# Performance work log

Measured on AMD Instinct MI355X. Metric: run time of the kernel, lower is better.

## Reference

```python
import jax, jax.numpy as jnp
import numpy as np

N_HEADS = 16
D_MODEL = 1024
HEAD_DIM = D_MODEL // N_HEADS
B, S = 2, 2048


def setup_inputs() -> dict:
    key = jax.random.key(0)
    ks = jax.random.split(key, 10)
    scale = 1.0 / np.sqrt(D_MODEL)
    inp = {
        "query_tokens": jax.random.normal(ks[0], (B, S, D_MODEL), dtype=jnp.float32),
        "key_or_value_tokens": jax.random.normal(ks[1], (B, S, D_MODEL), dtype=jnp.float32),
        "mask": jnp.ones((B, S, S), dtype=jnp.int32),
        "Wq": jax.random.normal(ks[2], (D_MODEL, D_MODEL), dtype=jnp.float32) * scale,
        "bq": jnp.zeros((D_MODEL,), dtype=jnp.float32),
        "Wk": jax.random.normal(ks[3], (D_MODEL, D_MODEL), dtype=jnp.float32) * scale,
        "bk": jnp.zeros((D_MODEL,), dtype=jnp.float32),
        "Wv": jax.random.normal(ks[4], (D_MODEL, D_MODEL), dtype=jnp.float32) * scale,
        "bv": jnp.zeros((D_MODEL,), dtype=jnp.float32),
        "Wo": jax.random.normal(ks[5], (D_MODEL, D_MODEL), dtype=jnp.float32) * scale,
        "bo": jnp.zeros((D_MODEL,), dtype=jnp.float32),
    }
    return inp


def reference(query_tokens, key_or_value_tokens, mask, Wq, bq, Wk, bk, Wv, bv, Wo, bo):
    b, s, d = query_tokens.shape
    h, dh = N_HEADS, HEAD_DIM

    def proj(x, W, bias):
        # torch Linear: x @ W.T + b ; then split heads -> (b, h, s, dh)
        y = jnp.einsum("bsd,ed->bse", x, W) + bias
        return y.reshape(b, -1, h, dh).transpose(0, 2, 1, 3)

    q = proj(query_tokens, Wq, bq)
    k = proj(key_or_value_tokens, Wk, bk)
    v = proj(key_or_value_tokens, Wv, bv)

    scores = jnp.einsum("bhqd,bhkd->bhqk", q, k) / jnp.sqrt(jnp.float32(dh))
    # mask: (b, Sq, Sk) -> (b, 1, Sq, Sk); zeros get large negative fill
    scores = jnp.where(mask[:, None, :, :] == 0, jnp.float32(-1e9), scores)
    attn = jax.nn.softmax(scores, axis=-1)
    out = jnp.einsum("bhqk,bhkd->bhqd", attn, v)
    out = out.transpose(0, 2, 1, 3).reshape(b, s, d)
    return jnp.einsum("bsd,ed->bse", out, Wo) + bo
```

## Files before the change

kernel.cpp:

```cpp
#include <hip/hip_runtime.h>
#include <hip/hip_bf16.h>

typedef __bf16 bf16_8  __attribute__((ext_vector_type(8)));
typedef __bf16 bf16_4  __attribute__((ext_vector_type(4)));
typedef float  f32_4   __attribute__((ext_vector_type(4)));

#define NH 16
#define DHD 64
#define BB 2
#define SS 2048
#define DD 1024

__device__ __forceinline__ void gload16(const __bf16* g, __bf16* l) {
    __builtin_amdgcn_global_load_lds(
        (const __attribute__((address_space(1))) void*)g,
        (__attribute__((address_space(3))) void*)l, 16, 0, 0);
}

__global__ __launch_bounds__(256) void conv_all(
    const float* __restrict__ s0, const float* __restrict__ s1,
    const float* __restrict__ s2, const float* __restrict__ s3,
    const float* __restrict__ s4, const float* __restrict__ s5,
    __bf16* __restrict__ d0, __bf16* __restrict__ d1, __bf16* __restrict__ d2,
    __bf16* __restrict__ d3, __bf16* __restrict__ d4, __bf16* __restrict__ d5) {
    const int y = blockIdx.y;
    if (y >= 2 && blockIdx.x >= 1024) return;
    const float* s = (y == 0) ? s0 : (y == 1) ? s1 : (y == 2) ? s2
                   : (y == 3) ? s3 : (y == 4) ? s4 : s5;
    __bf16* d      = (y == 0) ? d0 : (y == 1) ? d1 : (y == 2) ? d2
                   : (y == 3) ? d3 : (y == 4) ? d4 : d5;
    const int i = (blockIdx.x * 256 + threadIdx.x) * 4;
    f32_4 v = *(const f32_4*)&s[i];
    bf16_4 o; o[0] = (__bf16)v[0]; o[1] = (__bf16)v[1];
    o[2] = (__bf16)v[2]; o[3] = (__bf16)v[3];
    *(bf16_4*)&d[i] = o;
}

__global__ __launch_bounds__(256) void mask_flags_k(const int* __restrict__ mask,
                                                    int* __restrict__ flags) {
    const int id = blockIdx.x;
    const int b = id >> 10, qt = (id >> 5) & 31, kt = id & 31;
    const int t = threadIdx.x;
    const int row = t >> 2, seg = t & 3;
    const int* p = mask + ((size_t)b * SS + qt * 64 + row) * SS + kt * 64 + seg * 16;
    int any0 = 0;
#pragma unroll
    for (int i = 0; i < 4; ++i) {
        int4 v = *(const int4*)&p[i * 4];
        any0 |= (v.x == 0) | (v.y == 0) | (v.z == 0) | (v.w == 0);
    }
    unsigned long long bal = __ballot(any0);
    __shared__ int sf[4];
    if ((t & 63) == 0) sf[t >> 6] = (bal != 0ULL);
    __syncthreads();
    if (t == 0) flags[id] = sf[0] | sf[1] | sf[2] | sf[3];
}

template <int LAYOUT>
__device__ __forceinline__ void gemm_body(const __bf16* __restrict__ A,
                                          const __bf16* __restrict__ W,
                                          const float* __restrict__ bias,
                                          __bf16* __restrict__ out,
                                          __bf16* ldsA, __bf16* ldsB) {
    const int tid  = threadIdx.x;
    const int lane = tid & 63;
    const int w    = tid >> 6;
    const int quad = lane >> 4;
    const int l15  = lane & 15;
    const int wm   = (w >> 1) * 64;
    const int wn   = (w & 1) * 64;
    const int m0   = blockIdx.x * 128;
    const int n0   = blockIdx.y * 128;

    f32_4 acc[4][4] = {};

    for (int kt = 0; kt < 1024; kt += 32) {
#pragma unroll
        for (int cc = 0; cc < 2; ++cc) {
            const int c   = tid + cc * 256;
            const int row = c >> 2;
            const int cp  = c & 3;
            gload16(&A[(size_t)(m0 + row) * 1024 + kt + cp * 8], &ldsA[c * 8]);
            gload16(&W[(size_t)(n0 + row) * 1024 + kt + cp * 8], &ldsB[c * 8]);
        }
        __syncthreads();

        bf16_8 af[4], bfr[4];
#pragma unroll
        for (int i = 0; i < 4; ++i)
            af[i] = *(const bf16_8*)&ldsA[(wm + i * 16 + l15) * 32 + quad * 8];
#pragma unroll
        for (int j = 0; j < 4; ++j)
            bfr[j] = *(const bf16_8*)&ldsB[(wn + j * 16 + l15) * 32 + quad * 8];
#pragma unroll
        for (int i = 0; i < 4; ++i)
#pragma unroll
            for (int j = 0; j < 4; ++j)
                acc[i][j] = __builtin_amdgcn_mfma_f32_16x16x32_bf16(
                    af[i], bfr[j], acc[i][j], 0, 0, 0);
        __syncthreads();
    }

#pragma unroll
    for (int i = 0; i < 4; ++i) {
#pragma unroll
        for (int j = 0; j < 4; ++j) {
            const int col = n0 + wn + j * 16 + l15;
            const float bv = bias[col];
            if (LAYOUT == 2) {
                const int row0 = m0 + wm + i * 16 + quad * 4;
                bf16_4 pk;
#pragma unroll
                for (int r = 0; r < 4; ++r) pk[r] = (__bf16)(acc[i][j][r] + bv);
                const int bb = row0 >> 11, s0 = row0 & 2047;
                const int h = col >> 6, dh = col & 63;
                *(bf16_4*)&out[(((size_t)bb * NH + h) * DHD + dh) * SS + s0] = pk;
            } else {
#pragma unroll
                for (int r = 0; r < 4; ++r) {
                    const int row = m0 + wm + i * 16 + quad * 4 + r;
                    out[(((size_t)(row >> 11) * NH + (col >> 6)) * SS +
                         (row & 2047)) * DHD + (col & 63)] =
                        (__bf16)(acc[i][j][r] + bv);
                }
            }
        }
    }
}

__global__ __launch_bounds__(256) void gemm_qkv(
    const __bf16* __restrict__ Xq, const __bf16* __restrict__ Xkv,
    const __bf16* __restrict__ Wq, const float* __restrict__ bq,
    const __bf16* __restrict__ Wk, const float* __restrict__ bk,
    const __bf16* __restrict__ Wv, const float* __restrict__ bv,
    __bf16* __restrict__ Qo, __bf16* __restrict__ Ko, __bf16* __restrict__ VTo) {
    __shared__ __align__(16) __bf16 ldsA[128 * 32];
    __shared__ __align__(16) __bf16 ldsB[128 * 32];
    const int z = blockIdx.z;
    const __bf16* A    = (z == 0) ? Xq : Xkv;
    const __bf16* W    = (z == 0) ? Wq : (z == 1 ? Wk : Wv);
    const float* bias  = (z == 0) ? bq : (z == 1 ? bk : bv);
    if (z == 2)
        gemm_body<2>(A, W, bias, VTo, ldsA, ldsB);
    else
        gemm_body<0>(A, W, bias, (z == 0) ? Qo : Ko, ldsA, ldsB);
}

__global__ __launch_bounds__(256) void gemm_final(
    const __bf16* __restrict__ A, const __bf16* __restrict__ W,
    const float* __restrict__ bias, float* __restrict__ out) {
    __shared__ __align__(16) __bf16 ldsA[64 * 32];
    __shared__ __align__(16) __bf16 ldsB[64 * 32];
    const int tid  = threadIdx.x;
    const int lane = tid & 63;
    const int w    = tid >> 6;
    const int quad = lane >> 4;
    const int l15  = lane & 15;
    const int wm   = (w >> 1) * 32;
    const int wn   = (w & 1) * 32;
    const int m0   = blockIdx.x * 64;
    const int n0   = blockIdx.y * 64;

    const int isB = w >> 1;
    const __bf16* src = isB ? W : A;
    const int     bN  = isB ? n0 : m0;
    __bf16*       dst = isB ? ldsB : ldsA;
    const int     w2  = w & 1;

    f32_4 acc[2][2] = {};

    for (int kt = 0; kt < 1024; kt += 32) {
#pragma unroll
        for (int cc = 0; cc < 2; ++cc) {
            const int c   = w2 * 128 + cc * 64 + lane;
            const int row = c >> 2;
            const int cp  = c & 3;
            gload16(&src[(size_t)(bN + row) * 1024 + kt + cp * 8], &dst[c * 8]);
        }
        __syncthreads();

        bf16_8 af[2], bfr[2];
#pragma unroll
        for (int i = 0; i < 2; ++i)
            af[i] = *(const bf16_8*)&ldsA[(wm + i * 16 + l15) * 32 + quad * 8];
#pragma unroll
        for (int j = 0; j < 2; ++j)
            bfr[j] = *(const bf16_8*)&ldsB[(wn + j * 16 + l15) * 32 + quad * 8];
#pragma unroll
        for (int i = 0; i < 2; ++i)
#pragma unroll
            for (int j = 0; j < 2; ++j)
                acc[i][j] = __builtin_amdgcn_mfma_f32_16x16x32_bf16(
                    af[i], bfr[j], acc[i][j], 0, 0, 0);
        __syncthreads();
    }

#pragma unroll
    for (int i = 0; i < 2; ++i)
#pragma unroll
        for (int j = 0; j < 2; ++j) {
            const int col = n0 + wn + j * 16 + l15;
            const float bv = bias[col];
#pragma unroll
            for (int r = 0; r < 4; ++r) {
                const int row = m0 + wm + i * 16 + quad * 4 + r;
                out[(size_t)row * 1024 + col] = acc[i][j][r] + bv;
            }
        }
}

__global__ __launch_bounds__(256, 2) void flash_attn(
    const __bf16* __restrict__ Q, const __bf16* __restrict__ K,
    const __bf16* __restrict__ VT, const int* __restrict__ mask,
    const int* __restrict__ flags, __bf16* __restrict__ O) {
    __shared__ __align__(16) __bf16 ldsK[64 * 72];
    __shared__ __align__(16) __bf16 ldsVT[64 * 72];
    __shared__ __align__(16) __bf16 ldsP[128 * 72];

    const int tid  = threadIdx.x;
    const int lane = tid & 63;
    const int w    = tid >> 6;
    const int quad = lane >> 4;
    const int l15  = lane & 15;
    const int q0   = blockIdx.x * 128;
    const int bh   = blockIdx.y;
    const int b    = bh >> 4;

    const __bf16* Qb  = Q + (size_t)bh * SS * DHD;
    const __bf16* Kb  = K + (size_t)bh * SS * DHD;
    const __bf16* VTb = VT + (size_t)bh * DHD * SS;
    const int*    mb  = mask + (size_t)b * SS * SS;
    const int*    flb = flags + (size_t)b * 1024 + blockIdx.x * 64;

    bf16_8 qa[2][2];
#pragma unroll
    for (int mt = 0; mt < 2; ++mt)
#pragma unroll
        for (int ks = 0; ks < 2; ++ks) {
            bf16_8 t = *(const bf16_8*)&Qb[(size_t)(q0 + w * 32 + mt * 16 + l15) * DHD +
                                           ks * 32 + quad * 8];
#pragma unroll
            for (int e = 0; e < 8; ++e)
                qa[mt][ks][e] = (__bf16)((float)t[e] * 0.18033688011112042f);
        }

    f32_4 of[2][4] = {};
    float li[2][4] = {};

    const int r0 = tid >> 3;
    const int r1 = r0 + 32;
    const int cp = tid & 7;
    uint4 kr0 = *(const uint4*)&Kb[(size_t)r0 * DHD + cp * 8];
    uint4 kr1 = *(const uint4*)&Kb[(size_t)r1 * DHD + cp * 8];
    uint4 vr0 = *(const uint4*)&VTb[(size_t)r0 * SS + cp * 8];
    uint4 vr1 = *(const uint4*)&VTb[(size_t)r1 * SS + cp * 8];

    for (int k0 = 0; k0 < SS; k0 += 64) {
        *(uint4*)&ldsK[r0 * 72 + cp * 8]  = kr0;
        *(uint4*)&ldsK[r1 * 72 + cp * 8]  = kr1;
        *(uint4*)&ldsVT[r0 * 72 + cp * 8] = vr0;
        *(uint4*)&ldsVT[r1 * 72 + cp * 8] = vr1;
        if (k0 + 64 < SS) {
            const int kn = k0 + 64;
            kr0 = *(const uint4*)&Kb[(size_t)(kn + r0) * DHD + cp * 8];
            kr1 = *(const uint4*)&Kb[(size_t)(kn + r1) * DHD + cp * 8];
            vr0 = *(const uint4*)&VTb[(size_t)r0 * SS + kn + cp * 8];
            vr1 = *(const uint4*)&VTb[(size_t)r1 * SS + kn + cp * 8];
        }
        __syncthreads();

        const bool msk = ((flb[k0 >> 6] | flb[32 + (k0 >> 6)]) != 0);

        f32_4 sa[2][4] = {};
#pragma unroll
        for (int ks = 0; ks < 2; ++ks) {
            bf16_8 kb[4];
#pragma unroll
            for (int j = 0; j < 4; ++j)
                kb[j] = *(const bf16_8*)&ldsK[(j * 16 + l15) * 72 + ks * 32 + quad * 8];
#pragma unroll
            for (int mt = 0; mt < 2; ++mt)
#pragma unroll
                for (int j = 0; j < 4; ++j)
                    sa[mt][j] = __builtin_amdgcn_mfma_f32_16x16x32_bf16(
                        qa[mt][ks], kb[j], sa[mt][j], 0, 0, 0);
        }

        if (msk) {
#pragma unroll
            for (int mt = 0; mt < 2; ++mt)
#pragma unroll
                for (int j = 0; j < 4; ++j)
#pragma unroll
                    for (int r = 0; r < 4; ++r) {
                        const int qg = q0 + w * 32 + mt * 16 + quad * 4 + r;
                        const int kg = k0 + j * 16 + l15;
                        if (mb[(size_t)qg * SS + kg] == 0) sa[mt][j][r] = -1e9f;
                    }
        }

#pragma unroll
        for (int mt = 0; mt < 2; ++mt)
#pragma unroll
            for (int j = 0; j < 4; ++j)
#pragma unroll
                for (int r = 0; r < 4; ++r) {
                    const float p = exp2f(sa[mt][j][r]);
                    li[mt][r] += p;
                    ldsP[(w * 32 + mt * 16 + quad * 4 + r) * 72 + j * 16 + l15] =
                        (__bf16)p;
                }
        __syncthreads();

#pragma unroll
        for (int ks2 = 0; ks2 < 2; ++ks2) {
            bf16_8 pa[2], vb[4];
#pragma unroll
            for (int mt = 0; mt < 2; ++mt)
                pa[mt] = *(const bf16_8*)&ldsP[(w * 32 + mt * 16 + l15) * 72 +
                                               ks2 * 32 + quad * 8];
#pragma unroll
            for (int jo = 0; jo < 4; ++jo)
                vb[jo] = *(const bf16_8*)&ldsVT[(jo * 16 + l15) * 72 +
                                                ks2 * 32 + quad * 8];
#pragma unroll
            for (int mt = 0; mt < 2; ++mt)
#pragma unroll
                for (int jo = 0; jo < 4; ++jo)
                    of[mt][jo] = __builtin_amdgcn_mfma_f32_16x16x32_bf16(
                        pa[mt], vb[jo], of[mt][jo], 0, 0, 0);
        }
        __syncthreads();
    }

    const int hcol = (bh & 15) * 64;
#pragma unroll
    for (int mt = 0; mt < 2; ++mt)
#pragma unroll
        for (int r = 0; r < 4; ++r) {
            float ls = li[mt][r];
            ls += __shfl_xor(ls, 1);
            ls += __shfl_xor(ls, 2);
            ls += __shfl_xor(ls, 4);
            ls += __shfl_xor(ls, 8);
            const float inv = 1.0f / fmaxf(ls, 1e-37f);
            const int qg = q0 + w * 32 + mt * 16 + quad * 4 + r;
#pragma unroll
            for (int jo = 0; jo < 4; ++jo)
                O[((size_t)b * SS + qg) * DD + hcol + jo * 16 + l15] =
                    (__bf16)(of[mt][jo][r] * inv);
        }
}


extern "C" void kernel_launch(void* const* d_in, const int* in_sizes, int n_in,
                              void* d_out, int out_size, void* d_ws, size_t ws_size,
                              hipStream_t stream) {
    const float* xq   = (const float*)d_in[0];
    const float* xkv  = (const float*)d_in[1];
    const int*   mask = (const int*)d_in[2];
    const float* Wq   = (const float*)d_in[3];
    const float* bq   = (const float*)d_in[4];
    const float* Wk   = (const float*)d_in[5];
    const float* bk   = (const float*)d_in[6];
    const float* Wv   = (const float*)d_in[7];
    const float* bv   = (const float*)d_in[8];
    const float* Wo   = (const float*)d_in[9];
    const float* bo   = (const float*)d_in[10];

    __bf16* ws = (__bf16*)d_ws;
    const size_t big = (size_t)BB * SS * DD;
    const size_t wsz = (size_t)DD * DD;
    __bf16* Qw   = ws;
    __bf16* Kw   = Qw + big;
    __bf16* VTw  = Kw + big;
    __bf16* Aw   = VTw + big;
    __bf16* Xqb  = Aw + big;
    __bf16* Xkvb = Xqb + big;
    __bf16* Wqb  = Xkvb + big;
    __bf16* Wkb  = Wqb + wsz;
    __bf16* Wvb  = Wkb + wsz;
    __bf16* Wob  = Wvb + wsz;
    int* flags   = (int*)(Wob + wsz);

    conv_all<<<dim3(4096, 6), dim3(256), 0, stream>>>(xq, xkv, Wq, Wk, Wv, Wo,
                                                      Xqb, Xkvb, Wqb, Wkb, Wvb, Wob);
    mask_flags_k<<<dim3(2048), dim3(256), 0, stream>>>(mask, flags);
    gemm_qkv<<<dim3(32, 8, 3), dim3(256), 0, stream>>>(Xqb, Xkvb, Wqb, bq, Wkb, bk,
                                                       Wvb, bv, Qw, Kw, VTw);
    flash_attn<<<dim3(SS / 128, BB * NH), dim3(256), 0, stream>>>(Qw, Kw, VTw, mask,
                                                                  flags, Aw);
    gemm_final<<<dim3(64, 16), dim3(256), 0, stream>>>(Aw, Wob, bo, (float*)d_out);
}
```

Measured before the change: 270.4 us.

## Split attention work across eight waves and enlarge final GEMM row tile

The flash attention kernel now runs 512 threads per block, with each wave handling 16 query rows instead of 32. This halves per-wave accumulators and registers, raising the launch bound to allow more resident waves for latency hiding. The cost is that each wave reads K/V fragments from LDS for fewer rows, so LDS read traffic per MFMA doubles. Separately, the output projection GEMM moves to 128x64 tiles with each wave computing 32x64, which improves B-tile reuse but halves the block count.

```diff
diff --git a/kernel.cpp b/kernel.cpp
--- a/kernel.cpp
+++ b/kernel.cpp
@@ -149,47 +149,46 @@
 __global__ __launch_bounds__(256) void gemm_final(
     const __bf16* __restrict__ A, const __bf16* __restrict__ W,
     const float* __restrict__ bias, float* __restrict__ out) {
-    __shared__ __align__(16) __bf16 ldsA[64 * 32];
+    __shared__ __align__(16) __bf16 ldsA[128 * 32];
     __shared__ __align__(16) __bf16 ldsB[64 * 32];
     const int tid  = threadIdx.x;
     const int lane = tid & 63;
     const int w    = tid >> 6;
     const int quad = lane >> 4;
     const int l15  = lane & 15;
-    const int wm   = (w >> 1) * 32;
-    const int wn   = (w & 1) * 32;
-    const int m0   = blockIdx.x * 64;
+    const int wm   = w * 32;
+    const int m0   = blockIdx.x * 128;
     const int n0   = blockIdx.y * 64;
 
-    const int isB = w >> 1;
-    const __bf16* src = isB ? W : A;
-    const int     bN  = isB ? n0 : m0;
-    __bf16*       dst = isB ? ldsB : ldsA;
-    const int     w2  = w & 1;
-
-    f32_4 acc[2][2] = {};
+    f32_4 acc[2][4] = {};
 
     for (int kt = 0; kt < 1024; kt += 32) {
 #pragma unroll
         for (int cc = 0; cc < 2; ++cc) {
-            const int c   = w2 * 128 + cc * 64 + lane;
+            const int c   = tid + cc * 256;
             const int row = c >> 2;
             const int cp  = c & 3;
-            gload16(&src[(size_t)(bN + row) * 1024 + kt + cp * 8], &dst[c * 8]);
-        }
-        __syncthreads();
-
-        bf16_8 af[2], bfr[2];
+            gload16(&A[(size_t)(m0 + row) * 1024 + kt + cp * 8], &ldsA[c * 8]);
+        }
+        {
+            const int c   = tid;
+            const int row = c >> 2;
+            const int cp  = c & 3;
+            gload16(&W[(size_t)(n0 + row) * 1024 + kt + cp * 8], &ldsB[c * 8]);
+        }
+        __syncthreads();
+
+        bf16_8 af[2], bfr[4];
 #pragma unroll
         for (int i = 0; i < 2; ++i)
             af[i] = *(const bf16_8*)&ldsA[(wm + i * 16 + l15) * 32 + quad * 8];
 #pragma unroll
-        for (int j = 0; j < 2; ++j)
-            bfr[j] = *(const bf16_8*)&ldsB[(wn + j * 16 + l15) * 32 + quad * 8];
+        for (int j = 0; j < 4; ++j)
+            bfr[j] = *(const bf16_8*)&ldsB[(j * 16 + l15) * 32 + quad * 8];
 #pragma unroll
         for (int i = 0; i < 2; ++i)
 #pragma unroll
-            for (int j = 0; j < 2; ++j)
+            for (int j = 0; j < 4; ++j)
                 acc[i][j] = __builtin_amdgcn_mfma_f32_16x16x32_bf16(
                     af[i], bfr[j], acc[i][j], 0, 0, 0);
         __syncthreads();
@@ -198,8 +197,8 @@
 #pragma unroll
     for (int i = 0; i < 2; ++i)
 #pragma unroll
-        for (int j = 0; j < 2; ++j) {
-            const int col = n0 + wn + j * 16 + l15;
+        for (int j = 0; j < 4; ++j) {
+            const int col = n0 + j * 16 + l15;
             const float bv = bias[col];
 #pragma unroll
             for (int r = 0; r < 4; ++r) {
@@ -209,7 +208,7 @@
         }
 }
 
-__global__ __launch_bounds__(256, 2) void flash_attn(
+__global__ __launch_bounds__(512, 4) void flash_attn(
     const __bf16* __restrict__ Q, const __bf16* __restrict__ K,
     const __bf16* __restrict__ VT, const int* __restrict__ mask,
     const int* __restrict__ flags, __bf16* __restrict__ O) {
@@ -232,46 +231,37 @@
     const int*    mb  = mask + (size_t)b * SS * SS;
     const int*    flb = flags + (size_t)b * 1024 + blockIdx.x * 64;
 
-    bf16_8 qa[2][2];
-#pragma unroll
-    for (int mt = 0; mt < 2; ++mt)
-#pragma unroll
-        for (int ks = 0; ks < 2; ++ks) {
-            bf16_8 t = *(const bf16_8*)&Qb[(size_t)(q0 + w * 32 + mt * 16 + l15) * DHD +
-                                           ks * 32 + quad * 8];
-#pragma unroll
-            for (int e = 0; e < 8; ++e)
-                qa[mt][ks][e] = (__bf16)((float)t[e] * 0.18033688011112042f);
-        }
-
-    f32_4 of[2][4] = {};
-    float li[2][4] = {};
+    bf16_8 qa[2];
+#pragma unroll
+    for (int ks = 0; ks < 2; ++ks) {
+        bf16_8 t = *(const bf16_8*)&Qb[(size_t)(q0 + w * 16 + l15) * DHD +
+                                       ks * 32 + quad * 8];
+#pragma unroll
+        for (int e = 0; e < 8; ++e)
+            qa[ks][e] = (__bf16)((float)t[e] * 0.18033688011112042f);
+    }
+
+    f32_4 of[4] = {};
+    float li[4] = {};
 
     const int r0 = tid >> 3;
-    const int r1 = r0 + 32;
     const int cp = tid & 7;
-    uint4 kr0 = *(const uint4*)&Kb[(size_t)r0 * DHD + cp * 8];
-    uint4 kr1 = *(const uint4*)&Kb[(size_t)r1 * DHD + cp * 8];
-    uint4 vr0 = *(const uint4*)&VTb[(size_t)r0 * SS + cp * 8];
-    uint4 vr1 = *(const uint4*)&VTb[(size_t)r1 * SS + cp * 8];
+    uint4 kr = *(const uint4*)&Kb[(size_t)r0 * DHD + cp * 8];
+    uint4 vr = *(const uint4*)&VTb[(size_t)r0 * SS + cp * 8];
 
     for (int k0 = 0; k0 < SS; k0 += 64) {
-        *(uint4*)&ldsK[r0 * 72 + cp * 8]  = kr0;
-        *(uint4*)&ldsK[r1 * 72 + cp * 8]  = kr1;
-        *(uint4*)&ldsVT[r0 * 72 + cp * 8] = vr0;
-        *(uint4*)&ldsVT[r1 * 72 + cp * 8] = vr1;
+        *(uint4*)&ldsK[r0 * 72 + cp * 8]  = kr;
+        *(uint4*)&ldsVT[r0 * 72 + cp * 8] = vr;
         if (k0 + 64 < SS) {
             const int kn = k0 + 64;
-            kr0 = *(const uint4*)&Kb[(size_t)(kn + r0) * DHD + cp * 8];
-            kr1 = *(const uint4*)&Kb[(size_t)(kn + r1) * DHD + cp * 8];
-            vr0 = *(const uint4*)&VTb[(size_t)r0 * SS + kn + cp * 8];
-            vr1 = *(const uint4*)&VTb[(size_t)r1 * SS + kn + cp * 8];
+            kr = *(const uint4*)&Kb[(size_t)(kn + r0) * DHD + cp * 8];
+            vr = *(const uint4*)&VTb[(size_t)r0 * SS + kn + cp * 8];
         }
         __syncthreads();
 
         const bool msk = ((flb[k0 >> 6] | flb[32 + (k0 >> 6)]) != 0);
 
-        f32_4 sa[2][4] = {};
+        f32_4 sa[4] = {};
 #pragma unroll
         for (int ks = 0; ks < 2; ++ks) {
             bf16_8 kb[4];
@@ -279,77 +269,63 @@
             for (int j = 0; j < 4; ++j)
                 kb[j] = *(const bf16_8*)&ldsK[(j * 16 + l15) * 72 + ks * 32 + quad * 8];
 #pragma unroll
-            for (int mt = 0; mt < 2; ++mt)
-#pragma unroll
-                for (int j = 0; j < 4; ++j)
-                    sa[mt][j] = __builtin_amdgcn_mfma_f32_16x16x32_bf16(
-                        qa[mt][ks], kb[j], sa[mt][j], 0, 0, 0);
+            for (int j = 0; j < 4; ++j)
+                sa[j] = __builtin_amdgcn_mfma_f32_16x16x32_bf16(
+                    qa[ks], kb[j], sa[j], 0, 0, 0);
         }
 
         if (msk) {
 #pragma unroll
-            for (int mt = 0; mt < 2; ++mt)
-#pragma unroll
-                for (int j = 0; j < 4; ++j)
-#pragma unroll
-                    for (int r = 0; r < 4; ++r) {
-                        const int qg = q0 + w * 32 + mt * 16 + quad * 4 + r;
-                        const int kg = k0 + j * 16 + l15;
-                        if (mb[(size_t)qg * SS + kg] == 0) sa[mt][j][r] = -1e9f;
-                    }
-        }
-
-#pragma unroll
-        for (int mt = 0; mt < 2; ++mt)
-#pragma unroll
             for (int j = 0; j < 4; ++j)
 #pragma unroll
                 for (int r = 0; r < 4; ++r) {
-                    const float p = exp2f(sa[mt][j][r]);
-                    li[mt][r] += p;
-                    ldsP[(w * 32 + mt * 16 + quad * 4 + r) * 72 + j * 16 + l15] =
-                        (__bf16)p;
+                    const int qg = q0 + w * 16 + quad * 4 + r;
+                    const int kg = k0 + j * 16 + l15;
+                    if (mb[(size_t)qg * SS + kg] == 0) sa[j][r] = -1e9f;
                 }
+        }
+
+#pragma unroll
+        for (int j = 0; j < 4; ++j)
+#pragma unroll
+            for (int r = 0; r < 4; ++r) {
+                const float p = exp2f(sa[j][r]);
+                li[r] += p;
+                ldsP[(w * 16 + quad * 4 + r) * 72 + j * 16 + l15] = (__bf16)p;
+            }
         __syncthreads();
 
 #pragma unroll
         for (int ks2 = 0; ks2 < 2; ++ks2) {
-            bf16_8 pa[2], vb[4];
-#pragma unroll
-            for (int mt = 0; mt < 2; ++mt)
-                pa[mt] = *(const bf16_8*)&ldsP[(w * 32 + mt * 16 + l15) * 72 +
-                                               ks2 * 32 + quad * 8];
+            bf16_8 pa, vb[4];
+            pa = *(const bf16_8*)&ldsP[(w * 16 + l15) * 72 + ks2 * 32 + quad * 8];
 #pragma unroll
             for (int jo = 0; jo < 4; ++jo)
                 vb[jo] = *(const bf16_8*)&ldsVT[(jo * 16 + l15) * 72 +
                                                 ks2 * 32 + quad * 8];
 #pragma unroll
-            for (int mt = 0; mt < 2; ++mt)
-#pragma unroll
-                for (int jo = 0; jo < 4; ++jo)
-                    of[mt][jo] = __builtin_amdgcn_mfma_f32_16x16x32_bf16(
-                        pa[mt], vb[jo], of[mt][jo], 0, 0, 0);
+            for (int jo = 0; jo < 4; ++jo)
+                of[jo] = __builtin_amdgcn_mfma_f32_16x16x32_bf16(
+                    pa, vb[jo], of[jo], 0, 0, 0);
         }
         __syncthreads();
     }
 
     const int hcol = (bh & 15) * 64;
 #pragma unroll
-    for (int mt = 0; mt < 2; ++mt)
-#pragma unroll
-        for (int r = 0; r < 4; ++r) {
-            float ls = li[mt][r];
-            ls += __shfl_xor(ls, 1);
-            ls += __shfl_xor(ls, 2);
-            ls += __shfl_xor(ls, 4);
-            ls += __shfl_xor(ls, 8);
-            const float inv = 1.0f / fmaxf(ls, 1e-37f);
-            const int qg = q0 + w * 32 + mt * 16 + quad * 4 + r;
-#pragma unroll
-            for (int jo = 0; jo < 4; ++jo)
-                O[((size_t)b * SS + qg) * DD + hcol + jo * 16 + l15] =
-                    (__bf16)(of[mt][jo][r] * inv);
-        }
+    for (int r = 0; r < 4; ++r) {
+        float ls = li[r];
+        ls += __shfl_xor(ls, 1);
+        ls += __shfl_xor(ls, 2);
+        ls += __shfl_xor(ls, 4);
+        ls += __shfl_xor(ls, 8);
+        const float inv = 1.0f / fmaxf(ls, 1e-37f);
+        const int qg = q0 + w * 16 + quad * 4 + r;
+#pragma unroll
+        for (int jo = 0; jo < 4; ++jo)
+            O[((size_t)b * SS + qg) * DD + hcol + jo * 16 + l15] =
+                (__bf16)(of[jo][r] * inv);
+    }
 }
 
 
@@ -388,7 +364,7 @@
     mask_flags_k<<<dim3(2048), dim3(256), 0, stream>>>(mask, flags);
     gemm_qkv<<<dim3(32, 8, 3), dim3(256), 0, stream>>>(Xqb, Xkvb, Wqb, bq, Wkb, bk,
                                                        Wvb, bv, Qw, Kw, VTw);
-    flash_attn<<<dim3(SS / 128, BB * NH), dim3(256), 0, stream>>>(Qw, Kw, VTw, mask,
+    flash_attn<<<dim3(SS / 128, BB * NH), dim3(512), 0, stream>>>(Qw, Kw, VTw, mask,
                                                                   flags, Aw);
-    gemm_final<<<dim3(64, 16), dim3(256), 0, stream>>>(Aw, Wob, bo, (float*)d_out);
-}
+    gemm_final<<<dim3(32, 16), dim3(256), 0, stream>>>(Aw, Wob, bo, (float*)d_out);
+}
```

New measurement: 274.6 us. About the same (+1.6%).
